# Kernel optimization log

Hardware: AMD Instinct MI355X
Metric: run time of the kernel (lower is better)

The kernel has to match this reference:

```python
import jax, jax.numpy as jnp
import numpy as np


def setup_inputs() -> dict:
    key = jax.random.key(0)
    k1, k2, k3 = jax.random.split(key, 3)
    B, N, C, R = 256, 512, 1000, 64
    x = jax.random.normal(k1, (B, N), dtype=jnp.float32)
    # kaiming_uniform_(a=0) on weight [C, R, N]: bound = sqrt(6 / fan_in), fan_in = N
    bound = float(np.sqrt(6.0 / N))
    weight = jax.random.uniform(k2, (C, R, N), dtype=jnp.float32, minval=-bound, maxval=bound)
    # original inits bias to 0, but use random to exercise the subtraction path
    bias = jax.random.normal(k3, (C, N), dtype=jnp.float32) * 0.1
    return {"x": x, "weight": weight, "bias": bias}


def reference(x, weight, bias):
    # x: [B, N]; weight: [C, R, N]; bias: [C, N]
    # Faithful math: s_r[b, c] = W_c @ (x_b - bias_c);  out[b, c] = ||s_r[b, c]||^2
    # Fused form avoiding the [B, C, N] diff blowup:
    #   W_c (x_b - b_c) = (W x)_bc - (W b)_c
    Wx = jnp.einsum("bn,crn->bcr", x, weight)      # [B, C, R]
    Wb = jnp.einsum("cn,crn->cr", bias, weight)    # [C, R]
    s_r = Wx - Wb[None, :, :]                        # [B, C, R]
    out = jnp.sum(s_r * s_r, axis=-1)                # [B, C] squared L2 norm over r
    return out
```

## Files before the change

kernel.cpp:

```cpp
#include <hip/hip_runtime.h>
#include <hip/hip_bf16.h>

#define BDIM 256
#define NDIM 512
#define CDIM 1000
#define RDIM 64
#define BK 64
#define NT (NDIM / BK)

typedef __attribute__((ext_vector_type(4))) float f32x4;
typedef __attribute__((ext_vector_type(8))) short bf16x8;

__device__ __forceinline__ uint32_t pk2(float lo, float hi) {
    unsigned short l = __builtin_bit_cast(unsigned short, __float2bfloat16(lo));
    unsigned short h = __builtin_bit_cast(unsigned short, __float2bfloat16(hi));
    return ((uint32_t)h << 16) | (uint32_t)l;
}

__device__ __forceinline__ void gload16(const void* g, void* l) {
    __builtin_amdgcn_global_load_lds(
        (const __attribute__((address_space(1))) void*)g,
        (__attribute__((address_space(3))) void*)l, 16, 0, 0);
}

__global__ __launch_bounds__(256)
void Mahalanobis_xconv_kernel(const float* __restrict__ x, uint4* __restrict__ xws)
{
    const int tid = blockIdx.x * 256 + threadIdx.x;
    const int t   = tid >> 11;
    const int rem = tid & 2047;
    const int row = rem >> 3;
    const int sIn = (rem & 7) << 4;
    const int uIn = sIn ^ ((row & 7) << 4);
    const int col0 = t * BK + (uIn >> 1);
    const float4* src = reinterpret_cast<const float4*>(x + (size_t)row * NDIM + col0);
    const float4 a = src[0], b = src[1];
    uint4 pk = {pk2(a.x, a.y), pk2(a.z, a.w), pk2(b.x, b.y), pk2(b.z, b.w)};
    xws[tid] = pk;
}

__global__ __launch_bounds__(256, 4)
void Mahalanobis_72834055405642_kernel(const char* __restrict__ xws,
                                       const float* __restrict__ w,
                                       const float* __restrict__ bias,
                                       float* __restrict__ out)
{
    __shared__ alignas(16) char lds_x[BDIM * BK * 2];
    __shared__ alignas(16) char lds_w[RDIM * BK * 2];
    __shared__ float sb_lds[RDIM];

    const int tid  = threadIdx.x;
    const int lane = tid & 63;
    const int wv   = tid >> 6;
    const int l15  = lane & 15;
    const int lhi  = lane >> 4;
    const int c0   = blockIdx.x;

    const int jrow = tid >> 2;
    const int jq   = tid & 3;
    const float* wbase = w + (size_t)c0 * (RDIM * NDIM) + (size_t)jrow * NDIM + jq * 16;
    const float* bbase = bias + (size_t)c0 * NDIM + jq * 16;

    f32x4 acc[4][4];
    #pragma unroll
    for (int m = 0; m < 4; ++m)
        #pragma unroll
        for (int n = 0; n < 4; ++n)
            acc[m][n] = (f32x4){0.f, 0.f, 0.f, 0.f};

    float sbp = 0.f;
    const int swr = (l15 & 7) << 4;
    const int sww = (jrow & 7) << 4;

    for (int t = 0; t < NT; ++t) {
        const float4* wsrc = reinterpret_cast<const float4*>(wbase + t * BK);
        const float4* bsrc = reinterpret_cast<const float4*>(bbase + t * BK);
        float4 w0 = wsrc[0], w1 = wsrc[1], w2 = wsrc[2], w3 = wsrc[3];
        float4 b0 = bsrc[0], b1 = bsrc[1], b2 = bsrc[2], b3 = bsrc[3];

        #pragma unroll
        for (int q = 0; q < 8; ++q)
            gload16(xws + (size_t)t * 32768 + wv * 8192 + q * 1024 + lane * 16,
                    lds_x + wv * 8192 + q * 1024);

        sbp += w0.x*b0.x + w0.y*b0.y + w0.z*b0.z + w0.w*b0.w
             + w1.x*b1.x + w1.y*b1.y + w1.z*b1.z + w1.w*b1.w
             + w2.x*b2.x + w2.y*b2.y + w2.z*b2.z + w2.w*b2.w
             + w3.x*b3.x + w3.y*b3.y + w3.z*b3.z + w3.w*b3.w;
        {
            char* rowp = lds_w + jrow * 128;
            uint4 pa = {pk2(w0.x, w0.y), pk2(w0.z, w0.w), pk2(w1.x, w1.y), pk2(w1.z, w1.w)};
            uint4 pb = {pk2(w2.x, w2.y), pk2(w2.z, w2.w), pk2(w3.x, w3.y), pk2(w3.z, w3.w)};
            *reinterpret_cast<uint4*>(rowp + ((jq * 32) ^ sww))      = pa;
            *reinterpret_cast<uint4*>(rowp + ((jq * 32 + 16) ^ sww)) = pb;
        }

        __syncthreads();

        #pragma unroll
        for (int ks = 0; ks < 2; ++ks) {
            bf16x8 af[4];
            bf16x8 bfr[4];
            #pragma unroll
            for (int m = 0; m < 4; ++m) {
                const int row = wv * 64 + m * 16 + l15;
                af[m] = *reinterpret_cast<const bf16x8*>(
                    lds_x + row * 128 + ((ks * 64 + lhi * 16) ^ swr));
            }
            #pragma unroll
            for (int n = 0; n < 4; ++n) {
                const int row = n * 16 + l15;
                bfr[n] = *reinterpret_cast<const bf16x8*>(
                    lds_w + row * 128 + ((ks * 64 + lhi * 16) ^ swr));
            }
            #pragma unroll
            for (int m = 0; m < 4; ++m)
                #pragma unroll
                for (int n = 0; n < 4; ++n)
                    acc[m][n] = __builtin_amdgcn_mfma_f32_16x16x32_bf16(
                        af[m], bfr[n], acc[m][n], 0, 0, 0);
        }

        __syncthreads();
    }

    sbp += __shfl_xor(sbp, 1);
    sbp += __shfl_xor(sbp, 2);
    if (jq == 0) sb_lds[jrow] = sbp;
    __syncthreads();

    float sb[4];
    #pragma unroll
    for (int n = 0; n < 4; ++n) sb[n] = sb_lds[n * 16 + l15];

    #pragma unroll
    for (int m = 0; m < 4; ++m) {
        #pragma unroll
        for (int rg = 0; rg < 4; ++rg) {
            float p = 0.f;
            #pragma unroll
            for (int n = 0; n < 4; ++n) {
                const float d = acc[m][n][rg] - sb[n];
                p += d * d;
            }
            #pragma unroll
            for (int s = 1; s < 16; s <<= 1)
                p += __shfl_xor(p, s);
            if (l15 == 0) {
                const int b = wv * 64 + m * 16 + lhi * 4 + rg;
                out[(size_t)b * CDIM + c0] = p;
            }
        }
    }
}

__global__ __launch_bounds__(256, 2)
void Mahalanobis_fallback_kernel(const float* __restrict__ x,
                                 const float* __restrict__ w,
                                 const float* __restrict__ bias,
                                 float* __restrict__ out)
{
    __shared__ alignas(16) char lds_x[BDIM * BK * 2];
    __shared__ alignas(16) char lds_w[128 * BK * 2];
    __shared__ alignas(16) float bias_lds[2 * NDIM];
    __shared__ float sb_lds[128];

    const int tid  = threadIdx.x;
    const int lane = tid & 63;
    const int wv   = tid >> 6;
    const int l15  = lane & 15;
    const int lhi  = lane >> 4;
    const int c0   = blockIdx.x * 2;

    reinterpret_cast<float4*>(bias_lds)[tid] =
        reinterpret_cast<const float4*>(bias + (size_t)c0 * NDIM)[tid];

    f32x4 acc[4][8];
    #pragma unroll
    for (int m = 0; m < 4; ++m)
        #pragma unroll
        for (int n = 0; n < 8; ++n)
            acc[m][n] = (f32x4){0.f, 0.f, 0.f, 0.f};

    const int jrow = tid >> 1;
    const int jh   = tid & 1;
    const int cl   = jrow >> 6;
    const float* wbase  = w + (size_t)(c0 + cl) * (RDIM * NDIM)
                            + (size_t)(jrow & 63) * NDIM + jh * 32;
    const float* blbase = bias_lds + cl * NDIM + jh * 32;
    const int xrow = tid >> 2;
    const int xq   = tid & 3;

    float sbp = 0.f;
    __syncthreads();

    for (int kk = 0; kk < NDIM; kk += BK) {
        #pragma unroll
        for (int p = 0; p < 4; ++p) {
            const int r = p * 64 + xrow;
            const float4* src = reinterpret_cast<const float4*>(
                x + (size_t)r * NDIM + kk + xq * 16);
            float4 v0 = src[0], v1 = src[1], v2 = src[2], v3 = src[3];
            uint4 pa = {pk2(v0.x, v0.y), pk2(v0.z, v0.w), pk2(v1.x, v1.y), pk2(v1.z, v1.w)};
            uint4 pb = {pk2(v2.x, v2.y), pk2(v2.z, v2.w), pk2(v3.x, v3.y), pk2(v3.z, v3.w)};
            const int sw = (r & 7) << 4;
            char* rowp = lds_x + r * (BK * 2);
            *reinterpret_cast<uint4*>(rowp + ((xq * 32) ^ sw))      = pa;
            *reinterpret_cast<uint4*>(rowp + ((xq * 32 + 16) ^ sw)) = pb;
        }
        {
            const float4* src = reinterpret_cast<const float4*>(wbase + kk);
            const float4* bl  = reinterpret_cast<const float4*>(blbase + kk);
            char* rowp = lds_w + jrow * (BK * 2);
            const int sw = (jrow & 7) << 4;
            #pragma unroll
            for (int i2 = 0; i2 < 4; ++i2) {
                float4 va = src[i2 * 2];
                float4 vb = src[i2 * 2 + 1];
                float4 ba = bl[i2 * 2];
                float4 bb = bl[i2 * 2 + 1];
                sbp += va.x * ba.x + va.y * ba.y + va.z * ba.z + va.w * ba.w
                     + vb.x * bb.x + vb.y * bb.y + vb.z * bb.z + vb.w * bb.w;
                uint4 pkv = {pk2(va.x, va.y), pk2(va.z, va.w),
                             pk2(vb.x, vb.y), pk2(vb.z, vb.w)};
                *reinterpret_cast<uint4*>(rowp + ((jh * 64 + i2 * 16) ^ sw)) = pkv;
            }
        }
        __syncthreads();
        #pragma unroll
        for (int ks = 0; ks < 2; ++ks) {
            bf16x8 af[4];
            bf16x8 bfr[8];
            const int swr = (l15 & 7) << 4;
            #pragma unroll
            for (int m = 0; m < 4; ++m) {
                const int row = wv * 64 + m * 16 + l15;
                af[m] = *reinterpret_cast<const bf16x8*>(
                    lds_x + row * (BK * 2) + ((ks * 64 + lhi * 16) ^ swr));
            }
            #pragma unroll
            for (int n = 0; n < 8; ++n) {
                const int row = n * 16 + l15;
                bfr[n] = *reinterpret_cast<const bf16x8*>(
                    lds_w + row * (BK * 2) + ((ks * 64 + lhi * 16) ^ swr));
            }
            #pragma unroll
            for (int m = 0; m < 4; ++m)
                #pragma unroll
                for (int n = 0; n < 8; ++n)
                    acc[m][n] = __builtin_amdgcn_mfma_f32_16x16x32_bf16(
                        af[m], bfr[n], acc[m][n], 0, 0, 0);
        }
        __syncthreads();
    }

    sbp += __shfl_xor(sbp, 1);
    if (jh == 0) sb_lds[jrow] = sbp;
    __syncthreads();

    float sb[8];
    #pragma unroll
    for (int n = 0; n < 8; ++n) sb[n] = sb_lds[n * 16 + l15];

    #pragma unroll
    for (int m = 0; m < 4; ++m) {
        #pragma unroll
        for (int rg = 0; rg < 4; ++rg) {
            float p0 = 0.f, p1 = 0.f;
            #pragma unroll
            for (int n = 0; n < 4; ++n) {
                const float d0 = acc[m][n][rg]     - sb[n];
                const float d1 = acc[m][n + 4][rg] - sb[n + 4];
                p0 += d0 * d0;
                p1 += d1 * d1;
            }
            #pragma unroll
            for (int s = 1; s < 16; s <<= 1) {
                p0 += __shfl_xor(p0, s);
                p1 += __shfl_xor(p1, s);
            }
            if (l15 == 0) {
                const int b = wv * 64 + m * 16 + lhi * 4 + rg;
                float2 o2 = {p0, p1};
                *reinterpret_cast<float2*>(out + (size_t)b * CDIM + c0) = o2;
            }
        }
    }
}

extern "C" void kernel_launch(void* const* d_in, const int* in_sizes, int n_in,
                              void* d_out, int out_size, void* d_ws, size_t ws_size,
                              hipStream_t stream) {
    const float* x    = (const float*)d_in[0];
    const float* w    = (const float*)d_in[1];
    const float* bias = (const float*)d_in[2];
    float* out = (float*)d_out;

    if (ws_size >= (size_t)(BDIM * NDIM * 2)) {
        hipLaunchKernelGGL(Mahalanobis_xconv_kernel, dim3(64), dim3(256), 0, stream,
                           x, (uint4*)d_ws);
        hipLaunchKernelGGL(Mahalanobis_72834055405642_kernel, dim3(CDIM), dim3(256),
                           0, stream, (const char*)d_ws, w, bias, out);
    } else {
        hipLaunchKernelGGL(Mahalanobis_fallback_kernel, dim3(CDIM / 2), dim3(256),
                           0, stream, x, w, bias, out);
    }
}
```

Baseline: 50.81 us.

## Software-pipeline main kernel with double-buffered weight LDS and register prefetch

Restructures the main kernel's K loop into a software pipeline. Weight tiles are prefetched two steps ahead into alternating register sets with nontemporal loads, converted into a double-buffered LDS weight tile, and the next x tile is issued into LDS right after the A fragments are read. Bias is staged once in LDS, and MFMA blocks run under raised wave priority. It also swaps the fallback kernel for a single-class-per-block variant and lowers occupancy bounds from 4 to 3 blocks to fit the extra LDS and registers, accepting reduced occupancy and hand-written waitcnt/barrier ordering risk.

After: 59.94 us. +17.9%, slower.

```diff
diff --git a/kernel.cpp b/kernel.cpp
--- a/kernel.cpp
+++ b/kernel.cpp
@@ -39,14 +39,15 @@
     xws[tid] = pk;
 }
 
-__global__ __launch_bounds__(256, 4)
+__global__ __launch_bounds__(256, 3)
 void Mahalanobis_72834055405642_kernel(const char* __restrict__ xws,
                                        const float* __restrict__ w,
                                        const float* __restrict__ bias,
                                        float* __restrict__ out)
 {
     __shared__ alignas(16) char lds_x[BDIM * BK * 2];
-    __shared__ alignas(16) char lds_w[RDIM * BK * 2];
+    __shared__ alignas(16) char lds_w[2 * RDIM * BK * 2];
+    __shared__ alignas(16) float bias_lds[NDIM];
     __shared__ float sb_lds[RDIM];
 
     const int tid  = threadIdx.x;
@@ -59,6 +60,184 @@
     const int jrow = tid >> 2;
     const int jq   = tid & 3;
     const float* wbase = w + (size_t)c0 * (RDIM * NDIM) + (size_t)jrow * NDIM + jq * 16;
+
+    const int swr = (l15 & 7) << 4;
+    const int sww = (jrow & 7) << 4;
+
+    f32x4 acc[4][4];
+    #pragma unroll
+    for (int m = 0; m < 4; ++m)
+        #pragma unroll
+        for (int n = 0; n < 4; ++n)
+            acc[m][n] = (f32x4){0.f, 0.f, 0.f, 0.f};
+
+    float sbp = 0.f;
+    f32x4 wrA[4], wrB[4];
+
+    auto convW = [&](const f32x4* wr, int tt, char* dst) {
+        const f32x4* bl4 = reinterpret_cast<const f32x4*>(bias_lds + tt * BK + jq * 16);
+        const f32x4 b0 = bl4[0], b1 = bl4[1], b2 = bl4[2], b3 = bl4[3];
+        sbp += wr[0][0]*b0[0] + wr[0][1]*b0[1] + wr[0][2]*b0[2] + wr[0][3]*b0[3]
+             + wr[1][0]*b1[0] + wr[1][1]*b1[1] + wr[1][2]*b1[2] + wr[1][3]*b1[3]
+             + wr[2][0]*b2[0] + wr[2][1]*b2[1] + wr[2][2]*b2[2] + wr[2][3]*b2[3]
+             + wr[3][0]*b3[0] + wr[3][1]*b3[1] + wr[3][2]*b3[2] + wr[3][3]*b3[3];
+        char* rowp = dst + jrow * 128;
+        uint4 pa = {pk2(wr[0][0], wr[0][1]), pk2(wr[0][2], wr[0][3]),
+                    pk2(wr[1][0], wr[1][1]), pk2(wr[1][2], wr[1][3])};
+        uint4 pb = {pk2(wr[2][0], wr[2][1]), pk2(wr[2][2], wr[2][3]),
+                    pk2(wr[3][0], wr[3][1]), pk2(wr[3][2], wr[3][3])};
+        *reinterpret_cast<uint4*>(rowp + ((jq * 32) ^ sww))      = pa;
+        *reinterpret_cast<uint4*>(rowp + ((jq * 32 + 16) ^ sww)) = pb;
+    };
+
+    {
+        const float2 bv = *reinterpret_cast<const float2*>(bias + (size_t)c0 * NDIM + tid * 2);
+        *reinterpret_cast<float2*>(bias_lds + tid * 2) = bv;
+    }
+    #pragma unroll
+    for (int q = 0; q < 8; ++q)
+        gload16(xws + wv * 8192 + q * 1024 + lane * 16,
+                lds_x + wv * 8192 + q * 1024);
+    __builtin_amdgcn_sched_barrier(0);
+    {
+        const f32x4* s0 = reinterpret_cast<const f32x4*>(wbase);
+        #pragma unroll
+        for (int i = 0; i < 4; ++i) wrB[i] = __builtin_nontemporal_load(s0 + i);
+        const f32x4* s1 = reinterpret_cast<const f32x4*>(wbase + BK);
+        #pragma unroll
+        for (int i = 0; i < 4; ++i) wrA[i] = __builtin_nontemporal_load(s1 + i);
+    }
+    asm volatile("s_waitcnt lgkmcnt(0)" ::: "memory");
+    __builtin_amdgcn_s_barrier();
+    __builtin_amdgcn_sched_barrier(0);
+    convW(wrB, 0, lds_w);
+    asm volatile("s_waitcnt vmcnt(4) lgkmcnt(0)" ::: "memory");
+    __builtin_amdgcn_s_barrier();
+    __builtin_amdgcn_sched_barrier(0);
+
+    #pragma unroll
+    for (int t = 0; t < NT; ++t) {
+        char* ldsw_cur = lds_w + (t & 1) * 8192;
+        char* ldsw_nxt = lds_w + ((t & 1) ^ 1) * 8192;
+
+        bf16x8 af[4][2];
+        #pragma unroll
+        for (int m = 0; m < 4; ++m) {
+            const int row = wv * 64 + m * 16 + l15;
+            #pragma unroll
+            for (int ks = 0; ks < 2; ++ks)
+                af[m][ks] = *reinterpret_cast<const bf16x8*>(
+                    lds_x + row * 128 + ((ks * 64 + lhi * 16) ^ swr));
+        }
+
+        asm volatile("s_waitcnt lgkmcnt(0)" ::: "memory");
+        __builtin_amdgcn_sched_barrier(0);
+        __builtin_amdgcn_s_barrier();
+        __builtin_amdgcn_sched_barrier(0);
+
+        if (t < NT - 1) {
+            #pragma unroll
+            for (int q = 0; q < 8; ++q)
+                gload16(xws + (size_t)(t + 1) * 32768 + wv * 8192 + q * 1024 + lane * 16,
+                        lds_x + wv * 8192 + q * 1024);
+        }
+        __builtin_amdgcn_sched_barrier(0);
+        if (t < NT - 2) {
+            const f32x4* s = reinterpret_cast<const f32x4*>(wbase + (t + 2) * BK);
+            if ((t & 1) == 0) {
+                #pragma unroll
+                for (int i = 0; i < 4; ++i) wrB[i] = __builtin_nontemporal_load(s + i);
+            } else {
+                #pragma unroll
+                for (int i = 0; i < 4; ++i) wrA[i] = __builtin_nontemporal_load(s + i);
+            }
+        }
+
+        #pragma unroll
+        for (int ks = 0; ks < 2; ++ks) {
+            bf16x8 bfr[4];
+            #pragma unroll
+            for (int n = 0; n < 4; ++n) {
+                const int row = n * 16 + l15;
+                bfr[n] = *reinterpret_cast<const bf16x8*>(
+                    ldsw_cur + row * 128 + ((ks * 64 + lhi * 16) ^ swr));
+            }
+            __builtin_amdgcn_s_setprio(1);
+            #pragma unroll
+            for (int m = 0; m < 4; ++m)
+                #pragma unroll
+                for (int n = 0; n < 4; ++n)
+                    acc[m][n] = __builtin_amdgcn_mfma_f32_16x16x32_bf16(
+                        af[m][ks], bfr[n], acc[m][n], 0, 0, 0);
+            __builtin_amdgcn_s_setprio(0);
+        }
+
+        if (t < NT - 1) {
+            if ((t & 1) == 0) convW(wrA, t + 1, ldsw_nxt);
+            else              convW(wrB, t + 1, ldsw_nxt);
+        }
+
+        if (t < NT - 2) {
+            asm volatile("s_waitcnt vmcnt(4) lgkmcnt(0)" ::: "memory");
+            __builtin_amdgcn_s_barrier();
+            __builtin_amdgcn_sched_barrier(0);
+        } else if (t == NT - 2) {
+            asm volatile("s_waitcnt vmcnt(0) lgkmcnt(0)" ::: "memory");
+            __builtin_amdgcn_s_barrier();
+            __builtin_amdgcn_sched_barrier(0);
+        }
+    }
+
+    sbp += __shfl_xor(sbp, 1);
+    sbp += __shfl_xor(sbp, 2);
+    if (jq == 0) sb_lds[jrow] = sbp;
+    __syncthreads();
+
+    float sb[4];
+    #pragma unroll
+    for (int n = 0; n < 4; ++n) sb[n] = sb_lds[n * 16 + l15];
+
+    #pragma unroll
+    for (int m = 0; m < 4; ++m) {
+        #pragma unroll
+        for (int rg = 0; rg < 4; ++rg) {
+            float p = 0.f;
+            #pragma unroll
+            for (int n = 0; n < 4; ++n) {
+                const float d = acc[m][n][rg] - sb[n];
+                p += d * d;
+            }
+            #pragma unroll
+            for (int s = 1; s < 16; s <<= 1)
+                p += __shfl_xor(p, s);
+            if (l15 == 0) {
+                const int b = wv * 64 + m * 16 + lhi * 4 + rg;
+                out[(size_t)b * CDIM + c0] = p;
+            }
+        }
+    }
+}
+
+__global__ __launch_bounds__(256, 4)
+void Mahalanobis_fallback_kernel(const float* __restrict__ x,
+                                 const float* __restrict__ w,
+                                 const float* __restrict__ bias,
+                                 float* __restrict__ out)
+{
+    __shared__ alignas(16) char lds_x[BDIM * BK * 2];
+    __shared__ alignas(16) char lds_w[RDIM * BK * 2];
+    __shared__ float sb_lds[RDIM];
+
+    const int tid  = threadIdx.x;
+    const int lane = tid & 63;
+    const int wv   = tid >> 6;
+    const int l15  = lane & 15;
+    const int lhi  = lane >> 4;
+    const int c0   = blockIdx.x;
+
+    const int jrow = tid >> 2;
+    const int jq   = tid & 3;
+    const float* wbase = w + (size_t)c0 * (RDIM * NDIM) + (size_t)jrow * NDIM + jq * 16;
     const float* bbase = bias + (size_t)c0 * NDIM + jq * 16;
 
     f32x4 acc[4][4];
@@ -71,6 +250,8 @@
     float sbp = 0.f;
     const int swr = (l15 & 7) << 4;
     const int sww = (jrow & 7) << 4;
+    const int xrow = tid >> 2;
+    const int xq   = tid & 3;
 
     for (int t = 0; t < NT; ++t) {
         const float4* wsrc = reinterpret_cast<const float4*>(wbase + t * BK);
@@ -79,9 +260,18 @@
         float4 b0 = bsrc[0], b1 = bsrc[1], b2 = bsrc[2], b3 = bsrc[3];
 
         #pragma unroll
-        for (int q = 0; q < 8; ++q)
-            gload16(xws + (size_t)t * 32768 + wv * 8192 + q * 1024 + lane * 16,
-                    lds_x + wv * 8192 + q * 1024);
+        for (int p = 0; p < 4; ++p) {
+            const int r = p * 64 + xrow;
+            const float4* s = reinterpret_cast<const float4*>(
+                x + (size_t)r * NDIM + t * BK + xq * 16);
+            float4 va = s[0], vb = s[1], vc = s[2], vd = s[3];
+            uint4 pa = {pk2(va.x, va.y), pk2(va.z, va.w), pk2(vb.x, vb.y), pk2(vb.z, vb.w)};
+            uint4 pb = {pk2(vc.x, vc.y), pk2(vc.z, vc.w), pk2(vd.x, vd.y), pk2(vd.z, vd.w)};
+            const int sw = (r & 7) << 4;
+            char* rowp = lds_x + r * 128;
+            *reinterpret_cast<uint4*>(rowp + ((xq * 32) ^ sw))      = pa;
+            *reinterpret_cast<uint4*>(rowp + ((xq * 32 + 16) ^ sw)) = pb;
+        }
 
         sbp += w0.x*b0.x + w0.y*b0.y + w0.z*b0.z + w0.w*b0.w
              + w1.x*b1.x + w1.y*b1.y + w1.z*b1.z + w1.w*b1.w
@@ -154,140 +344,6 @@
     }
 }
 
-__global__ __launch_bounds__(256, 2)
-void Mahalanobis_fallback_kernel(const float* __restrict__ x,
-                                 const float* __restrict__ w,
-                                 const float* __restrict__ bias,
-                                 float* __restrict__ out)
-{
-    __shared__ alignas(16) char lds_x[BDIM * BK * 2];
-    __shared__ alignas(16) char lds_w[128 * BK * 2];
-    __shared__ alignas(16) float bias_lds[2 * NDIM];
-    __shared__ float sb_lds[128];
-
-    const int tid  = threadIdx.x;
-    const int lane = tid & 63;
-    const int wv   = tid >> 6;
-    const int l15  = lane & 15;
-    const int lhi  = lane >> 4;
-    const int c0   = blockIdx.x * 2;
-
-    reinterpret_cast<float4*>(bias_lds)[tid] =
-        reinterpret_cast<const float4*>(bias + (size_t)c0 * NDIM)[tid];
-
-    f32x4 acc[4][8];
-    #pragma unroll
-    for (int m = 0; m < 4; ++m)
-        #pragma unroll
-        for (int n = 0; n < 8; ++n)
-            acc[m][n] = (f32x4){0.f, 0.f, 0.f, 0.f};
-
-    const int jrow = tid >> 1;
-    const int jh   = tid & 1;
-    const int cl   = jrow >> 6;
-    const float* wbase  = w + (size_t)(c0 + cl) * (RDIM * NDIM)
-                            + (size_t)(jrow & 63) * NDIM + jh * 32;
-    const float* blbase = bias_lds + cl * NDIM + jh * 32;
-    const int xrow = tid >> 2;
-    const int xq   = tid & 3;
-
-    float sbp = 0.f;
-    __syncthreads();
-
-    for (int kk = 0; kk < NDIM; kk += BK) {
-        #pragma unroll
-        for (int p = 0; p < 4; ++p) {
-            const int r = p * 64 + xrow;
-            const float4* src = reinterpret_cast<const float4*>(
-                x + (size_t)r * NDIM + kk + xq * 16);
-            float4 v0 = src[0], v1 = src[1], v2 = src[2], v3 = src[3];
-            uint4 pa = {pk2(v0.x, v0.y), pk2(v0.z, v0.w), pk2(v1.x, v1.y), pk2(v1.z, v1.w)};
-            uint4 pb = {pk2(v2.x, v2.y), pk2(v2.z, v2.w), pk2(v3.x, v3.y), pk2(v3.z, v3.w)};
-            const int sw = (r & 7) << 4;
-            char* rowp = lds_x + r * (BK * 2);
-            *reinterpret_cast<uint4*>(rowp + ((xq * 32) ^ sw))      = pa;
-            *reinterpret_cast<uint4*>(rowp + ((xq * 32 + 16) ^ sw)) = pb;
-        }
-        {
-            const float4* src = reinterpret_cast<const float4*>(wbase + kk);
-            const float4* bl  = reinterpret_cast<const float4*>(blbase + kk);
-            char* rowp = lds_w + jrow * (BK * 2);
-            const int sw = (jrow & 7) << 4;
-            #pragma unroll
-            for (int i2 = 0; i2 < 4; ++i2) {
-                float4 va = src[i2 * 2];
-                float4 vb = src[i2 * 2 + 1];
-                float4 ba = bl[i2 * 2];
-                float4 bb = bl[i2 * 2 + 1];
-                sbp += va.x * ba.x + va.y * ba.y + va.z * ba.z + va.w * ba.w
-                     + vb.x * bb.x + vb.y * bb.y + vb.z * bb.z + vb.w * bb.w;
-                uint4 pkv = {pk2(va.x, va.y), pk2(va.z, va.w),
-                             pk2(vb.x, vb.y), pk2(vb.z, vb.w)};
-                *reinterpret_cast<uint4*>(rowp + ((jh * 64 + i2 * 16) ^ sw)) = pkv;
-            }
-        }
-        __syncthreads();
-        #pragma unroll
-        for (int ks = 0; ks < 2; ++ks) {
-            bf16x8 af[4];
-            bf16x8 bfr[8];
-            const int swr = (l15 & 7) << 4;
-            #pragma unroll
-            for (int m = 0; m < 4; ++m) {
-                const int row = wv * 64 + m * 16 + l15;
-                af[m] = *reinterpret_cast<const bf16x8*>(
-                    lds_x + row * (BK * 2) + ((ks * 64 + lhi * 16) ^ swr));
-            }
-            #pragma unroll
-            for (int n = 0; n < 8; ++n) {
-                const int row = n * 16 + l15;
-                bfr[n] = *reinterpret_cast<const bf16x8*>(
-                    lds_w + row * (BK * 2) + ((ks * 64 + lhi * 16) ^ swr));
-            }
-            #pragma unroll
-            for (int m = 0; m < 4; ++m)
-                #pragma unroll
-                for (int n = 0; n < 8; ++n)
-                    acc[m][n] = __builtin_amdgcn_mfma_f32_16x16x32_bf16(
-                        af[m], bfr[n], acc[m][n], 0, 0, 0);
-        }
-        __syncthreads();
-    }
-
-    sbp += __shfl_xor(sbp, 1);
-    if (jh == 0) sb_lds[jrow] = sbp;
-    __syncthreads();
-
-    float sb[8];
-    #pragma unroll
-    for (int n = 0; n < 8; ++n) sb[n] = sb_lds[n * 16 + l15];
-
-    #pragma unroll
-    for (int m = 0; m < 4; ++m) {
-        #pragma unroll
-        for (int rg = 0; rg < 4; ++rg) {
-            float p0 = 0.f, p1 = 0.f;
-            #pragma unroll
-            for (int n = 0; n < 4; ++n) {
-                const float d0 = acc[m][n][rg]     - sb[n];
-                const float d1 = acc[m][n + 4][rg] - sb[n + 4];
-                p0 += d0 * d0;
-                p1 += d1 * d1;
-            }
-            #pragma unroll
-            for (int s = 1; s < 16; s <<= 1) {
-                p0 += __shfl_xor(p0, s);
-                p1 += __shfl_xor(p1, s);
-            }
-            if (l15 == 0) {
-                const int b = wv * 64 + m * 16 + lhi * 4 + rg;
-                float2 o2 = {p0, p1};
-                *reinterpret_cast<float2*>(out + (size_t)b * CDIM + c0) = o2;
-            }
-        }
-    }
-}
-
 extern "C" void kernel_launch(void* const* d_in, const int* in_sizes, int n_in,
                               void* d_out, int out_size, void* d_ws, size_t ws_size,
                               hipStream_t stream) {
@@ -302,7 +358,7 @@
         hipLaunchKernelGGL(Mahalanobis_72834055405642_kernel, dim3(CDIM), dim3(256),
                            0, stream, (const char*)d_ws, w, bias, out);
     } else {
-        hipLaunchKernelGGL(Mahalanobis_fallback_kernel, dim3(CDIM / 2), dim3(256),
+        hipLaunchKernelGGL(Mahalanobis_fallback_kernel, dim3(CDIM), dim3(256),
                            0, stream, x, w, bias, out);
     }
 }
```

## Load MFMA operands directly from global memory, bypassing LDS staging

Applied to the files above, without the earlier changes.

The main kernel no longer stages x and W tiles through LDS with barriers. Each lane loads its MFMA fragments straight from global memory: bf16 x from a plain row-major workspace, and fp32 W, which is converted to bf16 in registers. The bias dot product is folded into per-lane partial sums reduced with shuffles. The loop is fully unrolled and launch bounds drop to 2 blocks per SM. This removes LDS traffic and syncs but relies on L2 reuse of x across blocks, makes global loads less coalesced, and may raise register pressure.

Measured after the change: 102.8 us. 102% more time.

```diff
diff --git a/kernel.cpp b/kernel.cpp
--- a/kernel.cpp
+++ b/kernel.cpp
@@ -10,6 +10,7 @@
 
 typedef __attribute__((ext_vector_type(4))) float f32x4;
 typedef __attribute__((ext_vector_type(8))) short bf16x8;
+typedef __attribute__((ext_vector_type(4))) unsigned int u32x4;
 
 __device__ __forceinline__ uint32_t pk2(float lo, float hi) {
     unsigned short l = __builtin_bit_cast(unsigned short, __float2bfloat16(lo));
@@ -17,38 +18,22 @@
     return ((uint32_t)h << 16) | (uint32_t)l;
 }
 
-__device__ __forceinline__ void gload16(const void* g, void* l) {
-    __builtin_amdgcn_global_load_lds(
-        (const __attribute__((address_space(1))) void*)g,
-        (__attribute__((address_space(3))) void*)l, 16, 0, 0);
-}
-
 __global__ __launch_bounds__(256)
-void Mahalanobis_xconv_kernel(const float* __restrict__ x, uint4* __restrict__ xws)
+void Mahalanobis_xconv_kernel(const float* __restrict__ x, u32x4* __restrict__ xbf)
 {
     const int tid = blockIdx.x * 256 + threadIdx.x;
-    const int t   = tid >> 11;
-    const int rem = tid & 2047;
-    const int row = rem >> 3;
-    const int sIn = (rem & 7) << 4;
-    const int uIn = sIn ^ ((row & 7) << 4);
-    const int col0 = t * BK + (uIn >> 1);
-    const float4* src = reinterpret_cast<const float4*>(x + (size_t)row * NDIM + col0);
-    const float4 a = src[0], b = src[1];
-    uint4 pk = {pk2(a.x, a.y), pk2(a.z, a.w), pk2(b.x, b.y), pk2(b.z, b.w)};
-    xws[tid] = pk;
-}
-
-__global__ __launch_bounds__(256, 4)
-void Mahalanobis_72834055405642_kernel(const char* __restrict__ xws,
+    const f32x4* src = reinterpret_cast<const f32x4*>(x) + (size_t)tid * 2;
+    const f32x4 a = src[0], b = src[1];
+    u32x4 pk = {pk2(a[0], a[1]), pk2(a[2], a[3]), pk2(b[0], b[1]), pk2(b[2], b[3])};
+    xbf[tid] = pk;
+}
+
+__global__ __launch_bounds__(256, 2)
+void Mahalanobis_72834055405642_kernel(const char* __restrict__ xbf,
                                        const float* __restrict__ w,
                                        const float* __restrict__ bias,
                                        float* __restrict__ out)
 {
-    __shared__ alignas(16) char lds_x[BDIM * BK * 2];
-    __shared__ alignas(16) char lds_w[RDIM * BK * 2];
-    __shared__ float sb_lds[RDIM];
-
     const int tid  = threadIdx.x;
     const int lane = tid & 63;
     const int wv   = tid >> 6;
@@ -56,6 +41,108 @@
     const int lhi  = lane >> 4;
     const int c0   = blockIdx.x;
 
+    const char* xb = xbf + (size_t)(wv * 64 + l15) * (NDIM * 2) + lhi * 16;
+    const float* wb = w + (size_t)c0 * (RDIM * NDIM) + (size_t)l15 * NDIM + lhi * 8;
+    const float* bb = bias + (size_t)c0 * NDIM + lhi * 8;
+
+    f32x4 acc[4][4];
+    #pragma unroll
+    for (int m = 0; m < 4; ++m)
+        #pragma unroll
+        for (int n = 0; n < 4; ++n)
+            acc[m][n] = (f32x4){0.f, 0.f, 0.f, 0.f};
+
+    float sbp[4] = {0.f, 0.f, 0.f, 0.f};
+
+    #pragma unroll
+    for (int t = 0; t < NT; ++t) {
+        #pragma unroll
+        for (int ks = 0; ks < 2; ++ks) {
+            const int ko = t * BK + ks * 32;
+
+            bf16x8 af[4];
+            #pragma unroll
+            for (int m = 0; m < 4; ++m)
+                af[m] = *reinterpret_cast<const bf16x8*>(
+                    xb + (size_t)m * 16 * (NDIM * 2) + ko * 2);
+
+            f32x4 wlo[4], whi[4];
+            #pragma unroll
+            for (int n = 0; n < 4; ++n) {
+                const f32x4* wp = reinterpret_cast<const f32x4*>(
+                    wb + (size_t)n * 16 * NDIM + ko);
+                wlo[n] = wp[0];
+                whi[n] = wp[1];
+            }
+
+            const f32x4* bp = reinterpret_cast<const f32x4*>(bb + ko);
+            const f32x4 blo = bp[0], bhi = bp[1];
+
+            bf16x8 bw[4];
+            #pragma unroll
+            for (int n = 0; n < 4; ++n) {
+                sbp[n] += wlo[n][0]*blo[0] + wlo[n][1]*blo[1]
+                        + wlo[n][2]*blo[2] + wlo[n][3]*blo[3]
+                        + whi[n][0]*bhi[0] + whi[n][1]*bhi[1]
+                        + whi[n][2]*bhi[2] + whi[n][3]*bhi[3];
+                u32x4 pk = {pk2(wlo[n][0], wlo[n][1]), pk2(wlo[n][2], wlo[n][3]),
+                            pk2(whi[n][0], whi[n][1]), pk2(whi[n][2], whi[n][3])};
+                bw[n] = __builtin_bit_cast(bf16x8, pk);
+            }
+
+            #pragma unroll
+            for (int m = 0; m < 4; ++m)
+                #pragma unroll
+                for (int n = 0; n < 4; ++n)
+                    acc[m][n] = __builtin_amdgcn_mfma_f32_16x16x32_bf16(
+                        af[m], bw[n], acc[m][n], 0, 0, 0);
+        }
+    }
+
+    #pragma unroll
+    for (int n = 0; n < 4; ++n) {
+        sbp[n] += __shfl_xor(sbp[n], 16);
+        sbp[n] += __shfl_xor(sbp[n], 32);
+    }
+
+    #pragma unroll
+    for (int m = 0; m < 4; ++m) {
+        #pragma unroll
+        for (int rg = 0; rg < 4; ++rg) {
+            float p = 0.f;
+            #pragma unroll
+            for (int n = 0; n < 4; ++n) {
+                const float d = acc[m][n][rg] - sbp[n];
+                p += d * d;
+            }
+            #pragma unroll
+            for (int s = 1; s < 16; s <<= 1)
+                p += __shfl_xor(p, s);
+            if (l15 == 0) {
+                const int b = wv * 64 + m * 16 + lhi * 4 + rg;
+                out[(size_t)b * CDIM + c0] = p;
+            }
+        }
+    }
+}
+
+__global__ __launch_bounds__(256, 4)
+void Mahalanobis_fallback_kernel(const float* __restrict__ x,
+                                 const float* __restrict__ w,
+                                 const float* __restrict__ bias,
+                                 float* __restrict__ out)
+{
+    __shared__ alignas(16) char lds_x[BDIM * BK * 2];
+    __shared__ alignas(16) char lds_w[RDIM * BK * 2];
+    __shared__ float sb_lds[RDIM];
+
+    const int tid  = threadIdx.x;
+    const int lane = tid & 63;
+    const int wv   = tid >> 6;
+    const int l15  = lane & 15;
+    const int lhi  = lane >> 4;
+    const int c0   = blockIdx.x;
+
     const int jrow = tid >> 2;
     const int jq   = tid & 3;
     const float* wbase = w + (size_t)c0 * (RDIM * NDIM) + (size_t)jrow * NDIM + jq * 16;
@@ -71,6 +158,8 @@
     float sbp = 0.f;
     const int swr = (l15 & 7) << 4;
     const int sww = (jrow & 7) << 4;
+    const int xrow = tid >> 2;
+    const int xq   = tid & 3;
 
     for (int t = 0; t < NT; ++t) {
         const float4* wsrc = reinterpret_cast<const float4*>(wbase + t * BK);
@@ -79,9 +168,18 @@
         float4 b0 = bsrc[0], b1 = bsrc[1], b2 = bsrc[2], b3 = bsrc[3];
 
         #pragma unroll
-        for (int q = 0; q < 8; ++q)
-            gload16(xws + (size_t)t * 32768 + wv * 8192 + q * 1024 + lane * 16,
-                    lds_x + wv * 8192 + q * 1024);
+        for (int p = 0; p < 4; ++p) {
+            const int r = p * 64 + xrow;
+            const float4* s = reinterpret_cast<const float4*>(
+                x + (size_t)r * NDIM + t * BK + xq * 16);
+            float4 va = s[0], vb = s[1], vc = s[2], vd = s[3];
+            uint4 pa = {pk2(va.x, va.y), pk2(va.z, va.w), pk2(vb.x, vb.y), pk2(vb.z, vb.w)};
+            uint4 pb = {pk2(vc.x, vc.y), pk2(vc.z, vc.w), pk2(vd.x, vd.y), pk2(vd.z, vd.w)};
+            const int sw = (r & 7) << 4;
+            char* rowp = lds_x + r * 128;
+            *reinterpret_cast<uint4*>(rowp + ((xq * 32) ^ sw))      = pa;
+            *reinterpret_cast<uint4*>(rowp + ((xq * 32 + 16) ^ sw)) = pb;
+        }
 
         sbp += w0.x*b0.x + w0.y*b0.y + w0.z*b0.z + w0.w*b0.w
              + w1.x*b1.x + w1.y*b1.y + w1.z*b1.z + w1.w*b1.w
@@ -154,140 +252,6 @@
     }
 }
 
-__global__ __launch_bounds__(256, 2)
-void Mahalanobis_fallback_kernel(const float* __restrict__ x,
-                                 const float* __restrict__ w,
-                                 const float* __restrict__ bias,
-                                 float* __restrict__ out)
-{
-    __shared__ alignas(16) char lds_x[BDIM * BK * 2];
-    __shared__ alignas(16) char lds_w[128 * BK * 2];
-    __shared__ alignas(16) float bias_lds[2 * NDIM];
-    __shared__ float sb_lds[128];
-
-    const int tid  = threadIdx.x;
-    const int lane = tid & 63;
-    const int wv   = tid >> 6;
-    const int l15  = lane & 15;
-    const int lhi  = lane >> 4;
-    const int c0   = blockIdx.x * 2;
-
-    reinterpret_cast<float4*>(bias_lds)[tid] =
-        reinterpret_cast<const float4*>(bias + (size_t)c0 * NDIM)[tid];
-
-    f32x4 acc[4][8];
-    #pragma unroll
-    for (int m = 0; m < 4; ++m)
-        #pragma unroll
-        for (int n = 0; n < 8; ++n)
-            acc[m][n] = (f32x4){0.f, 0.f, 0.f, 0.f};
-
-    const int jrow = tid >> 1;
-    const int jh   = tid & 1;
-    const int cl   = jrow >> 6;
-    const float* wbase  = w + (size_t)(c0 + cl) * (RDIM * NDIM)
-                            + (size_t)(jrow & 63) * NDIM + jh * 32;
-    const float* blbase = bias_lds + cl * NDIM + jh * 32;
-    const int xrow = tid >> 2;
-    const int xq   = tid & 3;
-
-    float sbp = 0.f;
-    __syncthreads();
-
-    for (int kk = 0; kk < NDIM; kk += BK) {
-        #pragma unroll
-        for (int p = 0; p < 4; ++p) {
-            const int r = p * 64 + xrow;
-            const float4* src = reinterpret_cast<const float4*>(
-                x + (size_t)r * NDIM + kk + xq * 16);
-            float4 v0 = src[0], v1 = src[1], v2 = src[2], v3 = src[3];
-            uint4 pa = {pk2(v0.x, v0.y), pk2(v0.z, v0.w), pk2(v1.x, v1.y), pk2(v1.z, v1.w)};
-            uint4 pb = {pk2(v2.x, v2.y), pk2(v2.z, v2.w), pk2(v3.x, v3.y), pk2(v3.z, v3.w)};
-            const int sw = (r & 7) << 4;
-            char* rowp = lds_x + r * (BK * 2);
-            *reinterpret_cast<uint4*>(rowp + ((xq * 32) ^ sw))      = pa;
-            *reinterpret_cast<uint4*>(rowp + ((xq * 32 + 16) ^ sw)) = pb;
-        }
-        {
-            const float4* src = reinterpret_cast<const float4*>(wbase + kk);
-            const float4* bl  = reinterpret_cast<const float4*>(blbase + kk);
-            char* rowp = lds_w + jrow * (BK * 2);
-            const int sw = (jrow & 7) << 4;
-            #pragma unroll
-            for (int i2 = 0; i2 < 4; ++i2) {
-                float4 va = src[i2 * 2];
-                float4 vb = src[i2 * 2 + 1];
-                float4 ba = bl[i2 * 2];
-                float4 bb = bl[i2 * 2 + 1];
-                sbp += va.x * ba.x + va.y * ba.y + va.z * ba.z + va.w * ba.w
-                     + vb.x * bb.x + vb.y * bb.y + vb.z * bb.z + vb.w * bb.w;
-                uint4 pkv = {pk2(va.x, va.y), pk2(va.z, va.w),
-                             pk2(vb.x, vb.y), pk2(vb.z, vb.w)};
-                *reinterpret_cast<uint4*>(rowp + ((jh * 64 + i2 * 16) ^ sw)) = pkv;
-            }
-        }
-        __syncthreads();
-        #pragma unroll
-        for (int ks = 0; ks < 2; ++ks) {
-            bf16x8 af[4];
-            bf16x8 bfr[8];
-            const int swr = (l15 & 7) << 4;
-            #pragma unroll
-            for (int m = 0; m < 4; ++m) {
-                const int row = wv * 64 + m * 16 + l15;
-                af[m] = *reinterpret_cast<const bf16x8*>(
-                    lds_x + row * (BK * 2) + ((ks * 64 + lhi * 16) ^ swr));
-            }
-            #pragma unroll
-            for (int n = 0; n < 8; ++n) {
-                const int row = n * 16 + l15;
-                bfr[n] = *reinterpret_cast<const bf16x8*>(
-                    lds_w + row * (BK * 2) + ((ks * 64 + lhi * 16) ^ swr));
-            }
-            #pragma unroll
-            for (int m = 0; m < 4; ++m)
-                #pragma unroll
-                for (int n = 0; n < 8; ++n)
-                    acc[m][n] = __builtin_amdgcn_mfma_f32_16x16x32_bf16(
-                        af[m], bfr[n], acc[m][n], 0, 0, 0);
-        }
-        __syncthreads();
-    }
-
-    sbp += __shfl_xor(sbp, 1);
-    if (jh == 0) sb_lds[jrow] = sbp;
-    __syncthreads();
-
-    float sb[8];
-    #pragma unroll
-    for (int n = 0; n < 8; ++n) sb[n] = sb_lds[n * 16 + l15];
-
-    #pragma unroll
-    for (int m = 0; m < 4; ++m) {
-        #pragma unroll
-        for (int rg = 0; rg < 4; ++rg) {
-            float p0 = 0.f, p1 = 0.f;
-            #pragma unroll
-            for (int n = 0; n < 4; ++n) {
-                const float d0 = acc[m][n][rg]     - sb[n];
-                const float d1 = acc[m][n + 4][rg] - sb[n + 4];
-                p0 += d0 * d0;
-                p1 += d1 * d1;
-            }
-            #pragma unroll
-            for (int s = 1; s < 16; s <<= 1) {
-                p0 += __shfl_xor(p0, s);
-                p1 += __shfl_xor(p1, s);
-            }
-            if (l15 == 0) {
-                const int b = wv * 64 + m * 16 + lhi * 4 + rg;
-                float2 o2 = {p0, p1};
-                *reinterpret_cast<float2*>(out + (size_t)b * CDIM + c0) = o2;
-            }
-        }
-    }
-}
-
 extern "C" void kernel_launch(void* const* d_in, const int* in_sizes, int n_in,
                               void* d_out, int out_size, void* d_ws, size_t ws_size,
                               hipStream_t stream) {
@@ -298,11 +262,11 @@
 
     if (ws_size >= (size_t)(BDIM * NDIM * 2)) {
         hipLaunchKernelGGL(Mahalanobis_xconv_kernel, dim3(64), dim3(256), 0, stream,
-                           x, (uint4*)d_ws);
+                           x, (u32x4*)d_ws);
         hipLaunchKernelGGL(Mahalanobis_72834055405642_kernel, dim3(CDIM), dim3(256),
                            0, stream, (const char*)d_ws, w, bias, out);
     } else {
-        hipLaunchKernelGGL(Mahalanobis_fallback_kernel, dim3(CDIM / 2), dim3(256),
+        hipLaunchKernelGGL(Mahalanobis_fallback_kernel, dim3(CDIM), dim3(256),
                            0, stream, x, w, bias, out);
     }
 }
```

## Process two classes per block with double-buffered weight tiles and prefetched x

Applied to the files above, without the earlier changes.

The main kernel now handles two classes per block, so each x tile loaded into LDS feeds a 256x128 MFMA tile instead of 256x64, halving x traffic per class. Weight tiles are double-buffered in LDS: the next tile's global loads are issued before the current MFMAs and converted to bf16 afterwards, and the next x tile is issued via global_load_lds once A fragments are in registers. Bias is staged in LDS and the bias dot product is accumulated per row. The cost is more registers and LDS per block (occupancy bound 2 instead of 4), and half as many blocks. The fallback kernel is rewritten as the old one-class kernel reading x directly.

After: 83.68 us. 64.7% more time.

```diff
diff --git a/kernel.cpp b/kernel.cpp
--- a/kernel.cpp
+++ b/kernel.cpp
@@ -39,11 +39,171 @@
     xws[tid] = pk;
 }
 
-__global__ __launch_bounds__(256, 4)
+__global__ __launch_bounds__(256, 2)
 void Mahalanobis_72834055405642_kernel(const char* __restrict__ xws,
                                        const float* __restrict__ w,
                                        const float* __restrict__ bias,
                                        float* __restrict__ out)
+{
+    __shared__ alignas(16) char  lds_x[BDIM * BK * 2];
+    __shared__ alignas(16) char  lds_w[2][128 * BK * 2];
+    __shared__ alignas(16) float bias_lds[2 * NDIM];
+    __shared__ float sb_lds[128];
+
+    const int tid  = threadIdx.x;
+    const int lane = tid & 63;
+    const int wv   = tid >> 6;
+    const int l15  = lane & 15;
+    const int lhi  = lane >> 4;
+    const int c0   = blockIdx.x * 2;
+
+    const int r0 = tid >> 4;
+    const int q  = tid & 15;
+    const float* wst = w + (size_t)c0 * (RDIM * NDIM) + (size_t)r0 * NDIM + q * 4;
+
+    const int swr = (l15 & 7) << 4;
+
+    f32x4 acc[4][8];
+    #pragma unroll
+    for (int m = 0; m < 4; ++m)
+        #pragma unroll
+        for (int n = 0; n < 8; ++n)
+            acc[m][n] = (f32x4){0.f, 0.f, 0.f, 0.f};
+
+    float sbq[8] = {0.f, 0.f, 0.f, 0.f, 0.f, 0.f, 0.f, 0.f};
+
+    auto loadW = [&](int t, f32x4* wr) {
+        #pragma unroll
+        for (int i = 0; i < 8; ++i)
+            wr[i] = *reinterpret_cast<const f32x4*>(wst + t * BK + (size_t)i * 16 * NDIM);
+    };
+    auto convW = [&](int t, const f32x4* wr, char* dst) {
+        #pragma unroll
+        for (int i = 0; i < 8; ++i) {
+            const int row = r0 + 16 * i;
+            const int cl  = row >> 6;
+            const f32x4 bv = *reinterpret_cast<const f32x4*>(
+                bias_lds + cl * NDIM + t * BK + q * 4);
+            sbq[i] += wr[i][0]*bv[0] + wr[i][1]*bv[1] + wr[i][2]*bv[2] + wr[i][3]*bv[3];
+            uint2 pk = {pk2(wr[i][0], wr[i][1]), pk2(wr[i][2], wr[i][3])};
+            *reinterpret_cast<uint2*>(dst + row * 128 + ((q * 8) ^ ((row & 7) << 4))) = pk;
+        }
+    };
+    auto issueX = [&](int t) {
+        #pragma unroll
+        for (int qq = 0; qq < 8; ++qq)
+            gload16(xws + (size_t)t * 32768 + wv * 8192 + qq * 1024 + (size_t)lane * 16,
+                    lds_x + wv * 8192 + qq * 1024);
+    };
+
+    {
+        const f32x4 bv = *reinterpret_cast<const f32x4*>(bias + (size_t)c0 * NDIM + tid * 4);
+        *reinterpret_cast<f32x4*>(bias_lds + tid * 4) = bv;
+    }
+    issueX(0);
+    {
+        f32x4 wr0[8];
+        loadW(0, wr0);
+        __syncthreads();
+        convW(0, wr0, lds_w[0]);
+        __syncthreads();
+    }
+
+    #pragma unroll
+    for (int t = 0; t < NT; ++t) {
+        char* wcur = lds_w[t & 1];
+        char* wnxt = lds_w[(t & 1) ^ 1];
+
+        f32x4 wr[8];
+        if (t < NT - 1) loadW(t + 1, wr);
+
+        bf16x8 af[4][2];
+        #pragma unroll
+        for (int m = 0; m < 4; ++m) {
+            const int row = wv * 64 + m * 16 + l15;
+            #pragma unroll
+            for (int ks = 0; ks < 2; ++ks)
+                af[m][ks] = *reinterpret_cast<const bf16x8*>(
+                    lds_x + row * 128 + ((ks * 64 + lhi * 16) ^ swr));
+        }
+
+        if (t < NT - 1) {
+            asm volatile("s_waitcnt lgkmcnt(0)" ::: "memory");
+            __builtin_amdgcn_sched_barrier(0);
+            issueX(t + 1);
+        }
+
+        #pragma unroll
+        for (int ks = 0; ks < 2; ++ks) {
+            bf16x8 bfr[8];
+            #pragma unroll
+            for (int n = 0; n < 8; ++n) {
+                const int row = n * 16 + l15;
+                bfr[n] = *reinterpret_cast<const bf16x8*>(
+                    wcur + row * 128 + ((ks * 64 + lhi * 16) ^ swr));
+            }
+            #pragma unroll
+            for (int m = 0; m < 4; ++m)
+                #pragma unroll
+                for (int n = 0; n < 8; ++n)
+                    acc[m][n] = __builtin_amdgcn_mfma_f32_16x16x32_bf16(
+                        af[m][ks], bfr[n], acc[m][n], 0, 0, 0);
+        }
+
+        if (t < NT - 1) convW(t + 1, wr, wnxt);
+
+        __syncthreads();
+    }
+
+    #pragma unroll
+    for (int i = 0; i < 8; ++i) {
+        sbq[i] += __shfl_xor(sbq[i], 1);
+        sbq[i] += __shfl_xor(sbq[i], 2);
+        sbq[i] += __shfl_xor(sbq[i], 4);
+        sbq[i] += __shfl_xor(sbq[i], 8);
+    }
+    if (q == 0) {
+        #pragma unroll
+        for (int i = 0; i < 8; ++i)
+            sb_lds[r0 + 16 * i] = sbq[i];
+    }
+    __syncthreads();
+
+    float sb[8];
+    #pragma unroll
+    for (int n = 0; n < 8; ++n) sb[n] = sb_lds[n * 16 + l15];
+
+    #pragma unroll
+    for (int m = 0; m < 4; ++m) {
+        #pragma unroll
+        for (int rg = 0; rg < 4; ++rg) {
+            float p0 = 0.f, p1 = 0.f;
+            #pragma unroll
+            for (int n = 0; n < 4; ++n) {
+                const float d0 = acc[m][n][rg]     - sb[n];
+                const float d1 = acc[m][n + 4][rg] - sb[n + 4];
+                p0 += d0 * d0;
+                p1 += d1 * d1;
+            }
+            #pragma unroll
+            for (int s = 1; s < 16; s <<= 1) {
+                p0 += __shfl_xor(p0, s);
+                p1 += __shfl_xor(p1, s);
+            }
+            if (l15 == 0) {
+                const int b = wv * 64 + m * 16 + lhi * 4 + rg;
+                float2 o2 = {p0, p1};
+                *reinterpret_cast<float2*>(out + (size_t)b * CDIM + c0) = o2;
+            }
+        }
+    }
+}
+
+__global__ __launch_bounds__(256, 4)
+void Mahalanobis_fallback_kernel(const float* __restrict__ x,
+                                 const float* __restrict__ w,
+                                 const float* __restrict__ bias,
+                                 float* __restrict__ out)
 {
     __shared__ alignas(16) char lds_x[BDIM * BK * 2];
     __shared__ alignas(16) char lds_w[RDIM * BK * 2];
@@ -71,6 +231,8 @@
     float sbp = 0.f;
     const int swr = (l15 & 7) << 4;
     const int sww = (jrow & 7) << 4;
+    const int xrow = tid >> 2;
+    const int xq   = tid & 3;
 
     for (int t = 0; t < NT; ++t) {
         const float4* wsrc = reinterpret_cast<const float4*>(wbase + t * BK);
@@ -79,9 +241,18 @@
         float4 b0 = bsrc[0], b1 = bsrc[1], b2 = bsrc[2], b3 = bsrc[3];
 
         #pragma unroll
-        for (int q = 0; q < 8; ++q)
-            gload16(xws + (size_t)t * 32768 + wv * 8192 + q * 1024 + lane * 16,
-                    lds_x + wv * 8192 + q * 1024);
+        for (int p = 0; p < 4; ++p) {
+            const int r = p * 64 + xrow;
+            const float4* s = reinterpret_cast<const float4*>(
+                x + (size_t)r * NDIM + t * BK + xq * 16);
+            float4 va = s[0], vb = s[1], vc = s[2], vd = s[3];
+            uint4 pa = {pk2(va.x, va.y), pk2(va.z, va.w), pk2(vb.x, vb.y), pk2(vb.z, vb.w)};
+            uint4 pb = {pk2(vc.x, vc.y), pk2(vc.z, vc.w), pk2(vd.x, vd.y), pk2(vd.z, vd.w)};
+            const int sw = (r & 7) << 4;
+            char* rowp = lds_x + r * 128;
+            *reinterpret_cast<uint4*>(rowp + ((xq * 32) ^ sw))      = pa;
+            *reinterpret_cast<uint4*>(rowp + ((xq * 32 + 16) ^ sw)) = pb;
+        }
 
         sbp += w0.x*b0.x + w0.y*b0.y + w0.z*b0.z + w0.w*b0.w
              + w1.x*b1.x + w1.y*b1.y + w1.z*b1.z + w1.w*b1.w
@@ -154,140 +325,6 @@
     }
 }
 
-__global__ __launch_bounds__(256, 2)
-void Mahalanobis_fallback_kernel(const float* __restrict__ x,
-                                 const float* __restrict__ w,
-                                 const float* __restrict__ bias,
-                                 float* __restrict__ out)
-{
-    __shared__ alignas(16) char lds_x[BDIM * BK * 2];
-    __shared__ alignas(16) char lds_w[128 * BK * 2];
-    __shared__ alignas(16) float bias_lds[2 * NDIM];
-    __shared__ float sb_lds[128];
-
-    const int tid  = threadIdx.x;
-    const int lane = tid & 63;
-    const int wv   = tid >> 6;
-    const int l15  = lane & 15;
-    const int lhi  = lane >> 4;
-    const int c0   = blockIdx.x * 2;
-
-    reinterpret_cast<float4*>(bias_lds)[tid] =
-        reinterpret_cast<const float4*>(bias + (size_t)c0 * NDIM)[tid];
-
-    f32x4 acc[4][8];
-    #pragma unroll
-    for (int m = 0; m < 4; ++m)
-        #pragma unroll
-        for (int n = 0; n < 8; ++n)
-            acc[m][n] = (f32x4){0.f, 0.f, 0.f, 0.f};
-
-    const int jrow = tid >> 1;
-    const int jh   = tid & 1;
-    const int cl   = jrow >> 6;
-    const float* wbase  = w + (size_t)(c0 + cl) * (RDIM * NDIM)
-                            + (size_t)(jrow & 63) * NDIM + jh * 32;
-    const float* blbase = bias_lds + cl * NDIM + jh * 32;
-    const int xrow = tid >> 2;
-    const int xq   = tid & 3;
-
-    float sbp = 0.f;
-    __syncthreads();
-
-    for (int kk = 0; kk < NDIM; kk += BK) {
-        #pragma unroll
-        for (int p = 0; p < 4; ++p) {
-            const int r = p * 64 + xrow;
-            const float4* src = reinterpret_cast<const float4*>(
-                x + (size_t)r * NDIM + kk + xq * 16);
-            float4 v0 = src[0], v1 = src[1], v2 = src[2], v3 = src[3];
-            uint4 pa = {pk2(v0.x, v0.y), pk2(v0.z, v0.w), pk2(v1.x, v1.y), pk2(v1.z, v1.w)};
-            uint4 pb = {pk2(v2.x, v2.y), pk2(v2.z, v2.w), pk2(v3.x, v3.y), pk2(v3.z, v3.w)};
-            const int sw = (r & 7) << 4;
-            char* rowp = lds_x + r * (BK * 2);
-            *reinterpret_cast<uint4*>(rowp + ((xq * 32) ^ sw))      = pa;
-            *reinterpret_cast<uint4*>(rowp + ((xq * 32 + 16) ^ sw)) = pb;
-        }
-        {
-            const float4* src = reinterpret_cast<const float4*>(wbase + kk);
-            const float4* bl  = reinterpret_cast<const float4*>(blbase + kk);
-            char* rowp = lds_w + jrow * (BK * 2);
-            const int sw = (jrow & 7) << 4;
-            #pragma unroll
-            for (int i2 = 0; i2 < 4; ++i2) {
-                float4 va = src[i2 * 2];
-                float4 vb = src[i2 * 2 + 1];
-                float4 ba = bl[i2 * 2];
-                float4 bb = bl[i2 * 2 + 1];
-                sbp += va.x * ba.x + va.y * ba.y + va.z * ba.z + va.w * ba.w
-                     + vb.x * bb.x + vb.y * bb.y + vb.z * bb.z + vb.w * bb.w;
-                uint4 pkv = {pk2(va.x, va.y), pk2(va.z, va.w),
-                             pk2(vb.x, vb.y), pk2(vb.z, vb.w)};
-                *reinterpret_cast<uint4*>(rowp + ((jh * 64 + i2 * 16) ^ sw)) = pkv;
-            }
-        }
-        __syncthreads();
-        #pragma unroll
-        for (int ks = 0; ks < 2; ++ks) {
-            bf16x8 af[4];
-            bf16x8 bfr[8];
-            const int swr = (l15 & 7) << 4;
-            #pragma unroll
-            for (int m = 0; m < 4; ++m) {
-                const int row = wv * 64 + m * 16 + l15;
-                af[m] = *reinterpret_cast<const bf16x8*>(
-                    lds_x + row * (BK * 2) + ((ks * 64 + lhi * 16) ^ swr));
-            }
-            #pragma unroll
-            for (int n = 0; n < 8; ++n) {
-                const int row = n * 16 + l15;
-                bfr[n] = *reinterpret_cast<const bf16x8*>(
-                    lds_w + row * (BK * 2) + ((ks * 64 + lhi * 16) ^ swr));
-            }
-            #pragma unroll
-            for (int m = 0; m < 4; ++m)
-                #pragma unroll
-                for (int n = 0; n < 8; ++n)
-                    acc[m][n] = __builtin_amdgcn_mfma_f32_16x16x32_bf16(
-                        af[m], bfr[n], acc[m][n], 0, 0, 0);
-        }
-        __syncthreads();
-    }
-
-    sbp += __shfl_xor(sbp, 1);
-    if (jh == 0) sb_lds[jrow] = sbp;
-    __syncthreads();
-
-    float sb[8];
-    #pragma unroll
-    for (int n = 0; n < 8; ++n) sb[n] = sb_lds[n * 16 + l15];
-
-    #pragma unroll
-    for (int m = 0; m < 4; ++m) {
-        #pragma unroll
-        for (int rg = 0; rg < 4; ++rg) {
-            float p0 = 0.f, p1 = 0.f;
-            #pragma unroll
-            for (int n = 0; n < 4; ++n) {
-                const float d0 = acc[m][n][rg]     - sb[n];
-                const float d1 = acc[m][n + 4][rg] - sb[n + 4];
-                p0 += d0 * d0;
-                p1 += d1 * d1;
-            }
-            #pragma unroll
-            for (int s = 1; s < 16; s <<= 1) {
-                p0 += __shfl_xor(p0, s);
-                p1 += __shfl_xor(p1, s);
-            }
-            if (l15 == 0) {
-                const int b = wv * 64 + m * 16 + lhi * 4 + rg;
-                float2 o2 = {p0, p1};
-                *reinterpret_cast<float2*>(out + (size_t)b * CDIM + c0) = o2;
-            }
-        }
-    }
-}
-
 extern "C" void kernel_launch(void* const* d_in, const int* in_sizes, int n_in,
                               void* d_out, int out_size, void* d_ws, size_t ws_size,
                               hipStream_t stream) {
@@ -299,10 +336,10 @@
     if (ws_size >= (size_t)(BDIM * NDIM * 2)) {
         hipLaunchKernelGGL(Mahalanobis_xconv_kernel, dim3(64), dim3(256), 0, stream,
                            x, (uint4*)d_ws);
-        hipLaunchKernelGGL(Mahalanobis_72834055405642_kernel, dim3(CDIM), dim3(256),
+        hipLaunchKernelGGL(Mahalanobis_72834055405642_kernel, dim3(CDIM / 2), dim3(256),
                            0, stream, (const char*)d_ws, w, bias, out);
     } else {
-        hipLaunchKernelGGL(Mahalanobis_fallback_kernel, dim3(CDIM / 2), dim3(256),
+        hipLaunchKernelGGL(Mahalanobis_fallback_kernel, dim3(CDIM), dim3(256),
                            0, stream, x, w, bias, out);
     }
 }
```
